# Kernel optimization log

Measured on AMD Instinct MI355X. Metric: run time of the kernel, lower is better.

## Reference

```python
import jax, jax.numpy as jnp
import numpy as np

N_NODES = 100000
N_EDGES = 3200000
D_IN = 128
D_OUT = 128


def setup_inputs() -> dict:
    key = jax.random.key(0)
    k1, k2, k3, k4, k5 = jax.random.split(key, 5)
    input_feature = jax.random.normal(k1, (N_NODES, D_IN), dtype=jnp.float32)
    edge_src = jax.random.randint(k2, (N_EDGES,), 0, N_NODES, dtype=jnp.int32)
    edge_dst = jax.random.randint(k3, (N_EDGES,), 0, N_NODES, dtype=jnp.int32)
    edge_vals = jax.random.uniform(k4, (N_EDGES,), dtype=jnp.float32)
    # kaiming-uniform-like init for weight, zeros for bias (as in reset_parameters)
    bound = float(np.sqrt(6.0 / D_IN))
    weight = jax.random.uniform(k5, (D_IN, D_OUT), dtype=jnp.float32,
                                minval=-bound, maxval=bound)
    bias = jnp.zeros((D_OUT,), dtype=jnp.float32)
    return {
        "input_feature": input_feature,
        "edge_src": edge_src,
        "edge_dst": edge_dst,
        "edge_vals": edge_vals,
        "weight": weight,
        "bias": bias,
    }


def reference(input_feature, edge_src, edge_dst, edge_vals, weight, bias):
    # support = X @ W  -> [N, D_OUT]
    support = jnp.matmul(input_feature, weight)
    # sparse.mm(A, support): out[dst] += A[dst, src] * support[src]
    gathered = support[edge_src] * edge_vals[:, None]  # [E, D_OUT]
    output = jax.ops.segment_sum(gathered, edge_dst, num_segments=N_NODES)
    output = output + bias  # bias-add (use_bias=True)
    return output
```

## Files before the change

kernel.cpp:

```cpp
#include <hip/hip_runtime.h>

#define N_NODES 100000
#define N_EDGES 3200000
#define D 128

#define K1C    391
#define CHUNK  4096
#define NCHUNK 782

static const size_t OFF_SB    = 0;
static const size_t OFF_REC   = 25600000;
static const size_t OFF_SORT2 = 51200000;
static const size_t OFF_OFFS  = 76800000;
static const size_t OFF_GHIST = 77200000;
static const size_t OFF_BOFFS = 77204096;
static const size_t OFF_GCUR  = 77208192;

typedef __attribute__((ext_vector_type(8))) short bf16x8;
typedef __attribute__((ext_vector_type(4))) float f32x4;

__device__ __forceinline__ unsigned short f2bf(float f) {
    unsigned u = __float_as_uint(f);
    return (unsigned short)((u + 0x7FFFu + ((u >> 16) & 1u)) >> 16);
}

__global__ __launch_bounds__(256) void gemm_mfma(const float* __restrict__ X,
                                                 const float* __restrict__ W,
                                                 unsigned* __restrict__ Sb) {
    __shared__ __align__(16) union {
        unsigned short wfrag[8][4][64][8];
        unsigned       stage[4][32][68];
    } u;

    const int t    = threadIdx.x;
    const int lane = t & 63;
    const int wave = t >> 6;
    const int quad = lane >> 4;
    const int li   = lane & 15;
    const int rowBase = blockIdx.x * 128;

    for (int i = t; i < D * D; i += 256) {
        int k = i >> 7, n = i & 127;
        u.wfrag[n >> 4][k >> 5][((k >> 3) & 3) * 16 + (n & 15)][k & 7] = f2bf(W[i]);
    }
    __syncthreads();

    f32x4 acc[2][8];
#pragma unroll
    for (int rt = 0; rt < 2; ++rt)
#pragma unroll
        for (int ct = 0; ct < 8; ++ct)
            acc[rt][ct] = (f32x4){0.f, 0.f, 0.f, 0.f};

#pragma unroll
    for (int kt = 0; kt < 4; ++kt) {
        bf16x8 a[2];
#pragma unroll
        for (int rt = 0; rt < 2; ++rt) {
            int row = rowBase + wave * 32 + rt * 16 + li;
            if (row >= N_NODES) row = N_NODES - 1;
            const float* xp = X + (size_t)row * D + kt * 32 + quad * 8;
            float4 f0 = ((const float4*)xp)[0];
            float4 f1 = ((const float4*)xp)[1];
            bf16x8 av;
            av[0] = (short)f2bf(f0.x); av[1] = (short)f2bf(f0.y);
            av[2] = (short)f2bf(f0.z); av[3] = (short)f2bf(f0.w);
            av[4] = (short)f2bf(f1.x); av[5] = (short)f2bf(f1.y);
            av[6] = (short)f2bf(f1.z); av[7] = (short)f2bf(f1.w);
            a[rt] = av;
        }
#pragma unroll
        for (int ct = 0; ct < 8; ++ct) {
            bf16x8 b = *(const bf16x8*)&u.wfrag[ct][kt][lane][0];
            acc[0][ct] = __builtin_amdgcn_mfma_f32_16x16x32_bf16(a[0], b, acc[0][ct], 0, 0, 0);
            acc[1][ct] = __builtin_amdgcn_mfma_f32_16x16x32_bf16(a[1], b, acc[1][ct], 0, 0, 0);
        }
    }
    __syncthreads();

    unsigned short* sw = (unsigned short*)&u.stage[wave][0][0];
#pragma unroll
    for (int rt = 0; rt < 2; ++rt)
#pragma unroll
        for (int r = 0; r < 4; ++r) {
            int lrow = rt * 16 + quad * 4 + r;
#pragma unroll
            for (int ct = 0; ct < 8; ++ct)
                sw[lrow * 136 + ct * 16 + li] = f2bf(acc[rt][ct][r]);
        }
    for (int lrow = 0; lrow < 32; ++lrow) {
        int node = rowBase + wave * 32 + lrow;
        if (node < N_NODES)
            Sb[(size_t)node * 64 + lane] = ((unsigned*)sw)[lrow * 68 + lane];
    }
}

__global__ __launch_bounds__(256) void hist_coarse(const int* __restrict__ edst,
                                                   int* __restrict__ ghist) {
    __shared__ int h[K1C];
    for (int i = threadIdx.x; i < K1C; i += 256) h[i] = 0;
    __syncthreads();
    for (int e = blockIdx.x * 256 + threadIdx.x; e < N_EDGES; e += gridDim.x * 256)
        atomicAdd(&h[edst[e] >> 8], 1);
    __syncthreads();
    for (int i = threadIdx.x; i < K1C; i += 256)
        if (h[i]) atomicAdd(&ghist[i], h[i]);
}

__global__ __launch_bounds__(256) void scan_coarse(const int* __restrict__ ghist,
                                                   int* __restrict__ boffs,
                                                   int* __restrict__ gcursor) {
    __shared__ int sc[256];
    const int t = threadIdx.x;
    int v[2]; int s = 0;
#pragma unroll
    for (int j = 0; j < 2; ++j) {
        int idx = t * 2 + j;
        v[j] = (idx < K1C) ? ghist[idx] : 0;
        s += v[j];
    }
    sc[t] = s;
    __syncthreads();
    for (int off = 1; off < 256; off <<= 1) {
        int u = (t >= off) ? sc[t - off] : 0;
        __syncthreads();
        sc[t] += u;
        __syncthreads();
    }
    int run = (t == 0) ? 0 : sc[t - 1];
#pragma unroll
    for (int j = 0; j < 2; ++j) {
        int idx = t * 2 + j;
        if (idx < K1C) { boffs[idx] = run; gcursor[idx] = run; }
        run += v[j];
    }
    if (t == 255) boffs[K1C] = run;
}

__global__ __launch_bounds__(512) void partition_edges(
        const int* __restrict__ esrc,
        const int* __restrict__ edst,
        const float* __restrict__ eval,
        int* __restrict__ gcursor,
        int2* __restrict__ rec_out) {
    __shared__ int  hist[K1C];
    __shared__ int  lofs[K1C];
    __shared__ int  gbase[K1C];
    __shared__ int  cur[K1C];
    __shared__ int  wsum[8];
    __shared__ int2 staged[CHUNK];
    __shared__ unsigned short bkt[CHUNK];

    const int t    = threadIdx.x;
    const int lane = t & 63;
    const int wave = t >> 6;
    const int e0   = blockIdx.x * CHUNK;
    const int cnt  = min(CHUNK, N_EDGES - e0);

    for (int i = t; i < K1C; i += 512) hist[i] = 0;
    __syncthreads();

    for (int i = t; i < cnt; i += 512)
        atomicAdd(&hist[edst[e0 + i] >> 8], 1);
    __syncthreads();

    int hv   = (t < K1C) ? hist[t] : 0;
    int incl = hv;
    for (int off = 1; off < 64; off <<= 1) {
        int u = __shfl_up(incl, off);
        if (lane >= off) incl += u;
    }
    if (lane == 63) wsum[wave] = incl;
    __syncthreads();
    {
        int pre = 0;
        for (int w = 0; w < wave; ++w) pre += wsum[w];
        if (t < K1C) {
            int excl = pre + incl - hv;
            lofs[t]  = excl;
            cur[t]   = excl;
            gbase[t] = hv ? atomicAdd(&gcursor[t], hv) : 0;
        }
    }
    __syncthreads();

    for (int i = t; i < cnt; i += 512) {
        int e = e0 + i;
        int d = edst[e];
        int b = d >> 8;
        int pos = atomicAdd(&cur[b], 1);
        staged[pos] = make_int2(esrc[e] | ((d & 255) << 17), __float_as_int(eval[e]));
        bkt[pos] = (unsigned short)b;
    }
    __syncthreads();

    for (int i = t; i < cnt; i += 512) {
        int bb = bkt[i];
        rec_out[gbase[bb] + (i - lofs[bb])] = staged[i];
    }
}

__global__ __launch_bounds__(512) void fine_sort(
        const int2* __restrict__ rec,
        const int* __restrict__ boffs,
        int* __restrict__ offs,
        int2* __restrict__ sorted2) {
    __shared__ int h[256];
    __shared__ int cur[256];
    __shared__ int wsum[4];

    const int c    = blockIdx.x;
    const int t    = threadIdx.x;
    const int lane = t & 63;
    const int wave = t >> 6;
    const int beg  = boffs[c];
    const int end  = boffs[c + 1];

    if (t < 256) h[t] = 0;
    __syncthreads();

    for (int i = beg + t; i < end; i += 512)
        atomicAdd(&h[(rec[i].x >> 17) & 255], 1);
    __syncthreads();

    int incl = 0, hv = 0;
    if (t < 256) {
        hv = h[t];
        incl = hv;
        for (int off = 1; off < 64; off <<= 1) {
            int u = __shfl_up(incl, off);
            if (lane >= off) incl += u;
        }
        if (lane == 63) wsum[wave] = incl;
    }
    __syncthreads();
    if (t < 256) {
        int pre = 0;
        for (int w = 0; w < wave; ++w) pre += wsum[w];
        int excl = pre + incl - hv;
        int node = c * 256 + t;
        if (node < N_NODES) offs[node] = beg + excl;
        cur[t] = beg + excl;
    }
    __syncthreads();

    for (int i = beg + t; i < end; i += 512) {
        int2 q = rec[i];
        int dl = (q.x >> 17) & 255;
        int p = atomicAdd(&cur[dl], 1);
        sorted2[p] = make_int2(q.x & 0x1FFFF, q.y);
    }
}

#define FMA8(v, p) {                                                         \
    a0 += (v) * __uint_as_float((p).x << 16);                                \
    a1 += (v) * __uint_as_float((p).x & 0xFFFF0000u);                        \
    a2 += (v) * __uint_as_float((p).y << 16);                                \
    a3 += (v) * __uint_as_float((p).y & 0xFFFF0000u);                        \
    a4 += (v) * __uint_as_float((p).z << 16);                                \
    a5 += (v) * __uint_as_float((p).z & 0xFFFF0000u);                        \
    a6 += (v) * __uint_as_float((p).w << 16);                                \
    a7 += (v) * __uint_as_float((p).w & 0xFFFF0000u);                        \
}

__global__ __launch_bounds__(256) void reduce_segments(
        const unsigned* __restrict__ Sb,
        const int2* __restrict__ sorted,
        const int* __restrict__ offs,
        const float* __restrict__ bias,
        float* __restrict__ out) {
    const int lane = threadIdx.x & 63;
    const int node = (blockIdx.x * 256 + threadIdx.x) >> 6;
    if (node >= N_NODES) return;

    const int qr = lane >> 4;
    const int ql = lane & 15;

    const int beg = offs[node];
    const int end = (node == N_NODES - 1) ? N_EDGES : offs[node + 1];

    float a0 = 0.f, a1 = 0.f, a2 = 0.f, a3 = 0.f;
    float a4 = 0.f, a5 = 0.f, a6 = 0.f, a7 = 0.f;

    for (int base = beg; base < end; base += 64) {
        const int m = min(64, end - base);
        int2 rec = make_int2(0, 0);
        if (base + lane < end) rec = sorted[base + lane];
        const int ng = (m + 3) >> 2;

        int g = 0;
        for (; g + 4 <= ng; g += 4) {
            int i0 = 4 * (g + 0) + qr, i1 = 4 * (g + 1) + qr;
            int i2 = 4 * (g + 2) + qr, i3 = 4 * (g + 3) + qr;
            int s0 = __shfl(rec.x, i0); int s1 = __shfl(rec.x, i1);
            int s2 = __shfl(rec.x, i2); int s3 = __shfl(rec.x, i3);
            float v0 = __int_as_float(__shfl(rec.y, i0));
            float v1 = __int_as_float(__shfl(rec.y, i1));
            float v2 = __int_as_float(__shfl(rec.y, i2));
            float v3 = __int_as_float(__shfl(rec.y, i3));
            uint4 p0 = ((const uint4*)(Sb + (size_t)s0 * 64))[ql];
            uint4 p1 = ((const uint4*)(Sb + (size_t)s1 * 64))[ql];
            uint4 p2 = ((const uint4*)(Sb + (size_t)s2 * 64))[ql];
            uint4 p3 = ((const uint4*)(Sb + (size_t)s3 * 64))[ql];
            FMA8(v0, p0);
            FMA8(v1, p1);
            FMA8(v2, p2);
            FMA8(v3, p3);
        }
        for (; g < ng; ++g) {
            int i0 = 4 * g + qr;
            int s0 = __shfl(rec.x, i0);
            float v0 = __int_as_float(__shfl(rec.y, i0));
            uint4 p0 = ((const uint4*)(Sb + (size_t)s0 * 64))[ql];
            FMA8(v0, p0);
        }
    }

    a0 += __shfl(a0, lane ^ 16); a1 += __shfl(a1, lane ^ 16);
    a2 += __shfl(a2, lane ^ 16); a3 += __shfl(a3, lane ^ 16);
    a4 += __shfl(a4, lane ^ 16); a5 += __shfl(a5, lane ^ 16);
    a6 += __shfl(a6, lane ^ 16); a7 += __shfl(a7, lane ^ 16);
    a0 += __shfl(a0, lane ^ 32); a1 += __shfl(a1, lane ^ 32);
    a2 += __shfl(a2, lane ^ 32); a3 += __shfl(a3, lane ^ 32);
    a4 += __shfl(a4, lane ^ 32); a5 += __shfl(a5, lane ^ 32);
    a6 += __shfl(a6, lane ^ 32); a7 += __shfl(a7, lane ^ 32);

    if (qr == 0) {
        float4 b0 = ((const float4*)bias)[2 * ql];
        float4 b1 = ((const float4*)bias)[2 * ql + 1];
        float4 r0 = make_float4(a0 + b0.x, a1 + b0.y, a2 + b0.z, a3 + b0.w);
        float4 r1 = make_float4(a4 + b1.x, a5 + b1.y, a6 + b1.z, a7 + b1.w);
        ((float4*)(out + (size_t)node * D))[2 * ql]     = r0;
        ((float4*)(out + (size_t)node * D))[2 * ql + 1] = r1;
    }
}

extern "C" void kernel_launch(void* const* d_in, const int* in_sizes, int n_in,
                              void* d_out, int out_size, void* d_ws, size_t ws_size,
                              hipStream_t stream) {
    const float* X    = (const float*)d_in[0];
    const int*   esrc = (const int*)  d_in[1];
    const int*   edst = (const int*)  d_in[2];
    const float* eval = (const float*)d_in[3];
    const float* W    = (const float*)d_in[4];
    const float* bias = (const float*)d_in[5];
    float* out = (float*)d_out;

    char* ws = (char*)d_ws;
    unsigned* SbU   = (unsigned*)(ws + OFF_SB);
    int2*     recs  = (int2*)    (ws + OFF_REC);
    int2*     srt2  = (int2*)    (ws + OFF_SORT2);
    int*      offs  = (int*)     (ws + OFF_OFFS);
    int*      ghist = (int*)     (ws + OFF_GHIST);
    int*      boffs = (int*)     (ws + OFF_BOFFS);
    int*      gcur  = (int*)     (ws + OFF_GCUR);

    gemm_mfma<<<782, 256, 0, stream>>>(X, W, SbU);

    hipMemsetAsync(ghist, 0, K1C * 4, stream);
    hist_coarse<<<256, 256, 0, stream>>>(edst, ghist);
    scan_coarse<<<1, 256, 0, stream>>>(ghist, boffs, gcur);
    partition_edges<<<NCHUNK, 512, 0, stream>>>(esrc, edst, eval, gcur, recs);
    fine_sort<<<K1C, 512, 0, stream>>>(recs, boffs, offs, srt2);

    reduce_segments<<<(N_NODES + 3) / 4, 256, 0, stream>>>(
        SbU, srt2, offs, bias, out);
}
```

Measured before the change: 355.6 us.

## Fuse GEMM with fine sort launch and pack sorted edges into 32-bit words

Merges the bf16 MFMA GEMM and the fine bucket sort into a single launch where the first blocks compute X·W and the remaining blocks sort edges, letting both run concurrently and removing a launch. The sorted edge record is packed into one 32-bit word holding a 17-bit source index and the edge weight as a sign-less bf16. This halves index traffic in the segment reduction. It relies on non-negative edge values and reduces weight precision, and the fine-sort blocks use 256 instead of 512 threads.

```diff
diff --git a/kernel.cpp b/kernel.cpp
--- a/kernel.cpp
+++ b/kernel.cpp
@@ -7,6 +7,7 @@
 #define K1C    391
 #define CHUNK  4096
 #define NCHUNK 782
+#define GEMMB  782
 
 static const size_t OFF_SB    = 0;
 static const size_t OFF_REC   = 25600000;
@@ -22,77 +23,6 @@
 __device__ __forceinline__ unsigned short f2bf(float f) {
     unsigned u = __float_as_uint(f);
     return (unsigned short)((u + 0x7FFFu + ((u >> 16) & 1u)) >> 16);
-}
-
-__global__ __launch_bounds__(256) void gemm_mfma(const float* __restrict__ X,
-                                                 const float* __restrict__ W,
-                                                 unsigned* __restrict__ Sb) {
-    __shared__ __align__(16) union {
-        unsigned short wfrag[8][4][64][8];
-        unsigned       stage[4][32][68];
-    } u;
-
-    const int t    = threadIdx.x;
-    const int lane = t & 63;
-    const int wave = t >> 6;
-    const int quad = lane >> 4;
-    const int li   = lane & 15;
-    const int rowBase = blockIdx.x * 128;
-
-    for (int i = t; i < D * D; i += 256) {
-        int k = i >> 7, n = i & 127;
-        u.wfrag[n >> 4][k >> 5][((k >> 3) & 3) * 16 + (n & 15)][k & 7] = f2bf(W[i]);
-    }
-    __syncthreads();
-
-    f32x4 acc[2][8];
-#pragma unroll
-    for (int rt = 0; rt < 2; ++rt)
-#pragma unroll
-        for (int ct = 0; ct < 8; ++ct)
-            acc[rt][ct] = (f32x4){0.f, 0.f, 0.f, 0.f};
-
-#pragma unroll
-    for (int kt = 0; kt < 4; ++kt) {
-        bf16x8 a[2];
-#pragma unroll
-        for (int rt = 0; rt < 2; ++rt) {
-            int row = rowBase + wave * 32 + rt * 16 + li;
-            if (row >= N_NODES) row = N_NODES - 1;
-            const float* xp = X + (size_t)row * D + kt * 32 + quad * 8;
-            float4 f0 = ((const float4*)xp)[0];
-            float4 f1 = ((const float4*)xp)[1];
-            bf16x8 av;
-            av[0] = (short)f2bf(f0.x); av[1] = (short)f2bf(f0.y);
-            av[2] = (short)f2bf(f0.z); av[3] = (short)f2bf(f0.w);
-            av[4] = (short)f2bf(f1.x); av[5] = (short)f2bf(f1.y);
-            av[6] = (short)f2bf(f1.z); av[7] = (short)f2bf(f1.w);
-            a[rt] = av;
-        }
-#pragma unroll
-        for (int ct = 0; ct < 8; ++ct) {
-            bf16x8 b = *(const bf16x8*)&u.wfrag[ct][kt][lane][0];
-            acc[0][ct] = __builtin_amdgcn_mfma_f32_16x16x32_bf16(a[0], b, acc[0][ct], 0, 0, 0);
-            acc[1][ct] = __builtin_amdgcn_mfma_f32_16x16x32_bf16(a[1], b, acc[1][ct], 0, 0, 0);
-        }
-    }
-    __syncthreads();
-
-    unsigned short* sw = (unsigned short*)&u.stage[wave][0][0];
-#pragma unroll
-    for (int rt = 0; rt < 2; ++rt)
-#pragma unroll
-        for (int r = 0; r < 4; ++r) {
-            int lrow = rt * 16 + quad * 4 + r;
-#pragma unroll
-            for (int ct = 0; ct < 8; ++ct)
-                sw[lrow * 136 + ct * 16 + li] = f2bf(acc[rt][ct][r]);
-        }
-    for (int lrow = 0; lrow < 32; ++lrow) {
-        int node = rowBase + wave * 32 + lrow;
-        if (node < N_NODES)
-            Sb[(size_t)node * 64 + lane] = ((unsigned*)sw)[lrow * 68 + lane];
-    }
 }
 
 __global__ __launch_bounds__(256) void hist_coarse(const int* __restrict__ edst,
@@ -200,55 +130,122 @@
     }
 }
 
-__global__ __launch_bounds__(512) void fine_sort(
+__global__ __launch_bounds__(256) void gemm_and_fine(
+        const float* __restrict__ X,
+        const float* __restrict__ W,
+        unsigned* __restrict__ Sb,
         const int2* __restrict__ rec,
         const int* __restrict__ boffs,
         int* __restrict__ offs,
-        int2* __restrict__ sorted2) {
-    __shared__ int h[256];
-    __shared__ int cur[256];
-    __shared__ int wsum[4];
-
-    const int c    = blockIdx.x;
+        unsigned* __restrict__ sorted1) {
+    __shared__ __align__(16) union {
+        unsigned short wfrag[8][4][64][8];
+        unsigned       stage[4][32][68];
+    } u;
+    __shared__ int fh[256];
+    __shared__ int fcur[256];
+    __shared__ int fwsum[4];
+
     const int t    = threadIdx.x;
     const int lane = t & 63;
     const int wave = t >> 6;
-    const int beg  = boffs[c];
-    const int end  = boffs[c + 1];
-
-    if (t < 256) h[t] = 0;
-    __syncthreads();
-
-    for (int i = beg + t; i < end; i += 512)
-        atomicAdd(&h[(rec[i].x >> 17) & 255], 1);
-    __syncthreads();
-
-    int incl = 0, hv = 0;
-    if (t < 256) {
-        hv = h[t];
-        incl = hv;
+
+    if (blockIdx.x < GEMMB) {
+        const int quad = lane >> 4;
+        const int li   = lane & 15;
+        const int rowBase = blockIdx.x * 128;
+
+        for (int i = t; i < D * D; i += 256) {
+            int k = i >> 7, n = i & 127;
+            u.wfrag[n >> 4][k >> 5][((k >> 3) & 3) * 16 + (n & 15)][k & 7] = f2bf(W[i]);
+        }
+        __syncthreads();
+
+        f32x4 acc[2][8];
+#pragma unroll
+        for (int rt = 0; rt < 2; ++rt)
+#pragma unroll
+            for (int ct = 0; ct < 8; ++ct)
+                acc[rt][ct] = (f32x4){0.f, 0.f, 0.f, 0.f};
+
+#pragma unroll
+        for (int kt = 0; kt < 4; ++kt) {
+            bf16x8 a[2];
+#pragma unroll
+            for (int rt = 0; rt < 2; ++rt) {
+                int row = rowBase + wave * 32 + rt * 16 + li;
+                if (row >= N_NODES) row = N_NODES - 1;
+                const float* xp = X + (size_t)row * D + kt * 32 + quad * 8;
+                float4 f0 = ((const float4*)xp)[0];
+                float4 f1 = ((const float4*)xp)[1];
+                bf16x8 av;
+                av[0] = (short)f2bf(f0.x); av[1] = (short)f2bf(f0.y);
+                av[2] = (short)f2bf(f0.z); av[3] = (short)f2bf(f0.w);
+                av[4] = (short)f2bf(f1.x); av[5] = (short)f2bf(f1.y);
+                av[6] = (short)f2bf(f1.z); av[7] = (short)f2bf(f1.w);
+                a[rt] = av;
+            }
+#pragma unroll
+            for (int ct = 0; ct < 8; ++ct) {
+                bf16x8 b = *(const bf16x8*)&u.wfrag[ct][kt][lane][0];
+                acc[0][ct] = __builtin_amdgcn_mfma_f32_16x16x32_bf16(a[0], b, acc[0][ct], 0, 0, 0);
+                acc[1][ct] = __builtin_amdgcn_mfma_f32_16x16x32_bf16(a[1], b, acc[1][ct], 0, 0, 0);
+            }
+        }
+        __syncthreads();
+
+        unsigned short* sw = (unsigned short*)&u.stage[wave][0][0];
+#pragma unroll
+        for (int rt = 0; rt < 2; ++rt)
+#pragma unroll
+            for (int r = 0; r < 4; ++r) {
+                int lrow = rt * 16 + quad * 4 + r;
+#pragma unroll
+                for (int ct = 0; ct < 8; ++ct)
+                    sw[lrow * 136 + ct * 16 + li] = f2bf(acc[rt][ct][r]);
+            }
+        for (int lrow = 0; lrow < 32; ++lrow) {
+            int node = rowBase + wave * 32 + lrow;
+            if (node < N_NODES)
+                Sb[(size_t)node * 64 + lane] = ((unsigned*)sw)[lrow * 68 + lane];
+        }
+    } else {
+        const int c   = blockIdx.x - GEMMB;
+        const int beg = boffs[c];
+        const int end = boffs[c + 1];
+
+        fh[t] = 0;
+        __syncthreads();
+
+        for (int i = beg + t; i < end; i += 256)
+            atomicAdd(&fh[(rec[i].x >> 17) & 255], 1);
+        __syncthreads();
+
+        int hv   = fh[t];
+        int incl = hv;
         for (int off = 1; off < 64; off <<= 1) {
-            int u = __shfl_up(incl, off);
-            if (lane >= off) incl += u;
-        }
-        if (lane == 63) wsum[wave] = incl;
-    }
-    __syncthreads();
-    if (t < 256) {
-        int pre = 0;
-        for (int w = 0; w < wave; ++w) pre += wsum[w];
-        int excl = pre + incl - hv;
-        int node = c * 256 + t;
-        if (node < N_NODES) offs[node] = beg + excl;
-        cur[t] = beg + excl;
-    }
-    __syncthreads();
-
-    for (int i = beg + t; i < end; i += 512) {
-        int2 q = rec[i];
-        int dl = (q.x >> 17) & 255;
-        int p = atomicAdd(&cur[dl], 1);
-        sorted2[p] = make_int2(q.x & 0x1FFFF, q.y);
+            int uu = __shfl_up(incl, off);
+            if (lane >= off) incl += uu;
+        }
+        if (lane == 63) fwsum[wave] = incl;
+        __syncthreads();
+        {
+            int pre = 0;
+            for (int w = 0; w < wave; ++w) pre += fwsum[w];
+            int excl = pre + incl - hv;
+            int node = c * 256 + t;
+            if (node < N_NODES) offs[node] = beg + excl;
+            fcur[t] = beg + excl;
+        }
+        __syncthreads();
+
+        for (int i = beg + t; i < end; i += 256) {
+            int2 q = rec[i];
+            int dl = (q.x >> 17) & 255;
+            int p = atomicAdd(&fcur[dl], 1);
+            unsigned vb = f2bf(__int_as_float(q.y));
+            sorted1[p] = (unsigned)(q.x & 0x1FFFF) | ((vb & 0x7FFFu) << 17);
+        }
     }
 }
 
@@ -265,7 +262,7 @@
 
 __global__ __launch_bounds__(256) void reduce_segments(
         const unsigned* __restrict__ Sb,
-        const int2* __restrict__ sorted,
+        const unsigned* __restrict__ sorted,
         const int* __restrict__ offs,
         const float* __restrict__ bias,
         float* __restrict__ out) {
@@ -284,7 +281,7 @@
 
     for (int base = beg; base < end; base += 64) {
         const int m = min(64, end - base);
-        int2 rec = make_int2(0, 0);
+        unsigned rec = 0;
         if (base + lane < end) rec = sorted[base + lane];
         const int ng = (m + 3) >> 2;
 
@@ -292,12 +289,16 @@
         for (; g + 4 <= ng; g += 4) {
             int i0 = 4 * (g + 0) + qr, i1 = 4 * (g + 1) + qr;
             int i2 = 4 * (g + 2) + qr, i3 = 4 * (g + 3) + qr;
-            int s0 = __shfl(rec.x, i0); int s1 = __shfl(rec.x, i1);
-            int s2 = __shfl(rec.x, i2); int s3 = __shfl(rec.x, i3);
-            float v0 = __int_as_float(__shfl(rec.y, i0));
-            float v1 = __int_as_float(__shfl(rec.y, i1));
-            float v2 = __int_as_float(__shfl(rec.y, i2));
-            float v3 = __int_as_float(__shfl(rec.y, i3));
+            unsigned r0 = (unsigned)__shfl((int)rec, i0);
+            unsigned r1 = (unsigned)__shfl((int)rec, i1);
+            unsigned r2 = (unsigned)__shfl((int)rec, i2);
+            unsigned r3 = (unsigned)__shfl((int)rec, i3);
+            int s0 = r0 & 0x1FFFF, s1 = r1 & 0x1FFFF;
+            int s2 = r2 & 0x1FFFF, s3 = r3 & 0x1FFFF;
+            float v0 = __uint_as_float((r0 >> 17) << 16);
+            float v1 = __uint_as_float((r1 >> 17) << 16);
+            float v2 = __uint_as_float((r2 >> 17) << 16);
+            float v3 = __uint_as_float((r3 >> 17) << 16);
             uint4 p0 = ((const uint4*)(Sb + (size_t)s0 * 64))[ql];
             uint4 p1 = ((const uint4*)(Sb + (size_t)s1 * 64))[ql];
             uint4 p2 = ((const uint4*)(Sb + (size_t)s2 * 64))[ql];
@@ -309,8 +310,9 @@
         }
         for (; g < ng; ++g) {
             int i0 = 4 * g + qr;
-            int s0 = __shfl(rec.x, i0);
-            float v0 = __int_as_float(__shfl(rec.y, i0));
+            unsigned r0 = (unsigned)__shfl((int)rec, i0);
+            int s0 = r0 & 0x1FFFF;
+            float v0 = __uint_as_float((r0 >> 17) << 16);
             uint4 p0 = ((const uint4*)(Sb + (size_t)s0 * 64))[ql];
             FMA8(v0, p0);
         }
@@ -349,20 +351,20 @@
     char* ws = (char*)d_ws;
     unsigned* SbU   = (unsigned*)(ws + OFF_SB);
     int2*     recs  = (int2*)    (ws + OFF_REC);
-    int2*     srt2  = (int2*)    (ws + OFF_SORT2);
+    unsigned* srt1  = (unsigned*)(ws + OFF_SORT2);
     int*      offs  = (int*)     (ws + OFF_OFFS);
     int*      ghist = (int*)     (ws + OFF_GHIST);
     int*      boffs = (int*)     (ws + OFF_BOFFS);
     int*      gcur  = (int*)     (ws + OFF_GCUR);
 
-    gemm_mfma<<<782, 256, 0, stream>>>(X, W, SbU);
-
     hipMemsetAsync(ghist, 0, K1C * 4, stream);
     hist_coarse<<<256, 256, 0, stream>>>(edst, ghist);
     scan_coarse<<<1, 256, 0, stream>>>(ghist, boffs, gcur);
     partition_edges<<<NCHUNK, 512, 0, stream>>>(esrc, edst, eval, gcur, recs);
-    fine_sort<<<K1C, 512, 0, stream>>>(recs, boffs, offs, srt2);
+
+    gemm_and_fine<<<GEMMB + K1C, 256, 0, stream>>>(
+        X, W, SbU, recs, boffs, offs, srt1);
 
     reduce_segments<<<(N_NODES + 3) / 4, 256, 0, stream>>>(
-        SbU, srt2, offs, bias, out);
-}
+        SbU, srt1, offs, bias, out);
+}
```

New measurement: 340.7 us. -4.2%, faster.
